# Kernel tuning notes

Measured on AMD Instinct MI355X. Metric: run time of the kernel, lower is better.

## Reference

```python
import jax, jax.numpy as jnp
import numpy as np

B, S, D = 4, 2048, 1024

def setup_inputs() -> dict:
    key = jax.random.key(0)
    k1, k2, k3, k4 = jax.random.split(key, 4)
    x = jax.random.normal(k1, (B, S, D), dtype=jnp.float32)
    # module init: jr.normal(key, (dim, dim)) / 40
    Qw = jax.random.normal(k2, (D, D), dtype=jnp.float32) / 40
    Kw = jax.random.normal(k3, (D, D), dtype=jnp.float32) / 40
    Vw = jax.random.normal(k4, (D, D), dtype=jnp.float32) / 40
    return {"x": x, "Qw": Qw, "Kw": Kw, "Vw": Vw}

def reference(x, Qw, Kw, Vw):
    # Q/K/V projections: [B,S,D] @ [D,D] -> [B,S,D]
    Q = x @ Qw
    K = x @ Kw
    V = x @ Vw
    d = x.shape[-1]
    S_len = x.shape[-2]
    # causal additive mask: 0 on/below diagonal, -inf above
    mask = jnp.where(jnp.tril(jnp.ones((S_len, S_len), dtype=x.dtype)) == 0,
                     -jnp.inf, 0.0).astype(x.dtype)
    # scores: [B,S,S]
    scores = jnp.einsum('bqd,bkd->bqk', Q, K) / jnp.sqrt(jnp.asarray(d, x.dtype))
    scores = scores + mask
    attn = jax.nn.softmax(scores, axis=-1)
    return jnp.einsum('bqk,bkd->bqd', attn, V)
```

## Files before the change

### kernel.cpp

```cpp
#include <hip/hip_runtime.h>
#include <hip/hip_bf16.h>

typedef __attribute__((ext_vector_type(8))) __bf16 bf16x8;
typedef __attribute__((ext_vector_type(8))) short short8;
typedef __attribute__((ext_vector_type(4))) float f32x4;

#define BM 128
#define BN 128
#define BK 64

__device__ inline unsigned short f2bf(float f) {
    union { float f; unsigned u; } v; v.f = f;
    unsigned r = (v.u + 0x7FFFu + ((v.u >> 16) & 1u)) >> 16;
    return (unsigned short)r;
}

__device__ __forceinline__ void gld16(const void* g, void* l) {
    __builtin_amdgcn_global_load_lds(
        (const __attribute__((address_space(1))) unsigned int*)g,
        (__attribute__((address_space(3))) unsigned int*)l, 16, 0, 0);
}

__global__ void detect_dtype(const unsigned short* __restrict__ x, int* __restrict__ flag)
{
    const int tid = threadIdx.x;
    int cnt = 0;
    for (int i = tid; i < 1024; i += 256) {
        unsigned e = (x[2 * i] >> 7) & 0xFFu;
        cnt += (e >= 0x60u && e <= 0x88u) ? 1 : 0;
    }
    #pragma unroll
    for (int o = 32; o >= 1; o >>= 1) cnt += __shfl_xor(cnt, o, 64);
    __shared__ int red[4];
    if ((tid & 63) == 0) red[tid >> 6] = cnt;
    __syncthreads();
    if (tid == 0) {
        int t = red[0] + red[1] + red[2] + red[3];
        *flag = (t >= 512) ? 0 : 1;
    }
}

__global__ __launch_bounds__(256, 2)
void gemm_bt(const unsigned short* __restrict__ A, const unsigned short* __restrict__ Bt,
             void* __restrict__ Call, int K, int lda, int ldb, int ldc,
             long oA, long oB, long oC, long sA, long sB, long sC,
             float scale, int mode, int q0,
             const int* __restrict__ dtf, int outKind)
{
    const int dt = *dtf;
    const int z = blockIdx.z;
    const long aBase = oA + (long)z * sA;
    const long bBase = oB + (long)z * sB;
    const long cBase = oC + (long)z * sC;

    int mt, nt;
    if (mode == 2) {
        const int nwg2 = gridDim.x * gridDim.y;
        const int h = blockIdx.y * gridDim.x + blockIdx.x;
        const int u = h >> 1;
        const int rank = (h & 1) ? (nwg2 - 1 - u) : u;
        mt = (gridDim.y - 1) - (rank / (int)gridDim.x);
        nt = rank % (int)gridDim.x;
    } else {
        const int nwg = gridDim.x * gridDim.y;
        int lin = blockIdx.y * gridDim.x + blockIdx.x;
        const int q = nwg >> 3, r = nwg & 7;
        const int xcd = lin & 7, idx = lin >> 3;
        lin = (xcd < r ? xcd * (q + 1) : r * (q + 1) + (xcd - r) * q) + idx;
        if (mode == 1) {
            int rem = lin, rr = 0, w = q0 / BN + 1;
            while (rem >= w) { rem -= w; rr++; w++; }
            mt = rr; nt = rem;
        } else { mt = lin / gridDim.x; nt = lin % gridDim.x; }
    }
    const int m0 = mt * BM;
    const int n0 = nt * BN;
    int kmax = K;
    if (mode == 2) kmax = min(K, q0 + m0 + BM);

    __shared__ __align__(16) short As[2][BM * BK];
    __shared__ __align__(16) short Bs[2][BN * BK];

    const int tid  = threadIdx.x;
    const int wave = tid >> 6;
    const int lane = tid & 63;
    const int wm = (wave >> 1) * 64;
    const int wn = (wave & 1) * 64;
    const int lrow = lane & 15;
    const int quad = lane >> 4;

    const int sRow = lane >> 3;
    const int sCol = ((lane & 7) ^ sRow) * 8;
    const long gA = aBase + (long)(m0 + wave * 32 + sRow) * lda + sCol;
    const long gB = bBase + (long)(n0 + wave * 32 + sRow) * ldb + sCol;

    auto stage = [&](int buf, int k0) {
        short* dA = &As[buf][wave * 32 * BK];
        short* dB = &Bs[buf][wave * 32 * BK];
        const unsigned short* pA = A + gA + k0;
        const unsigned short* pB = Bt + gB + k0;
        #pragma unroll
        for (int c = 0; c < 4; c++) {
            gld16(pA + (long)(c * 8) * lda, dA + c * 8 * BK);
            gld16(pB + (long)(c * 8) * ldb, dB + c * 8 * BK);
        }
    };

    f32x4 acc[4][4];
    #pragma unroll
    for (int i = 0; i < 4; i++)
        #pragma unroll
        for (int j = 0; j < 4; j++) {
            f32x4 zero = {0.f, 0.f, 0.f, 0.f};
            acc[i][j] = zero;
        }

    const int rq  = lrow & 7;
    const int pc0 = (quad ^ rq) * 8;
    const int pc1 = ((quad + 4) ^ rq) * 8;

    stage(0, 0);
    __syncthreads();
    int cur = 0;

    for (int k0 = 0; k0 < kmax; k0 += BK) {
        const int kn = k0 + BK;
        if (kn < kmax) stage(cur ^ 1, kn);

        const short* rA = &As[cur][0];
        const short* rB = &Bs[cur][0];
        bf16x8 af[4], bfr[4];
        #pragma unroll
        for (int i = 0; i < 4; i++) {
            af[i]  = *(const bf16x8*)&rA[(wm + i * 16 + lrow) * BK + pc0];
            bfr[i] = *(const bf16x8*)&rB[(wn + i * 16 + lrow) * BK + pc0];
        }
        #pragma unroll
        for (int i = 0; i < 4; i++)
            #pragma unroll
            for (int j = 0; j < 4; j++)
                acc[i][j] = __builtin_amdgcn_mfma_f32_16x16x32_bf16(af[i], bfr[j], acc[i][j], 0, 0, 0);
        #pragma unroll
        for (int i = 0; i < 4; i++) {
            af[i]  = *(const bf16x8*)&rA[(wm + i * 16 + lrow) * BK + pc1];
            bfr[i] = *(const bf16x8*)&rB[(wn + i * 16 + lrow) * BK + pc1];
        }
        #pragma unroll
        for (int i = 0; i < 4; i++)
            #pragma unroll
            for (int j = 0; j < 4; j++)
                acc[i][j] = __builtin_amdgcn_mfma_f32_16x16x32_bf16(af[i], bfr[j], acc[i][j], 0, 0, 0);

        __syncthreads();
        cur ^= 1;
    }

    const int oF32 = (outKind == 1) | ((outKind == 2) & dt);
    #pragma unroll
    for (int i = 0; i < 4; i++) {
        const int mr = m0 + wm + i * 16 + quad * 4;
        #pragma unroll
        for (int j = 0; j < 4; j++) {
            const int nc = n0 + wn + j * 16 + lrow;
            #pragma unroll
            for (int r = 0; r < 4; r++) {
                const long ofs = cBase + (long)(mr + r) * ldc + nc;
                const float v = acc[i][j][r] * scale;
                if (oF32) ((float*)Call)[ofs] = v;
                else      ((unsigned short*)Call)[ofs] = f2bf(v);
            }
        }
    }
}

__global__ __launch_bounds__(256)
void xpose_cast(const void* __restrict__ src, unsigned short* __restrict__ dT,
                unsigned short* __restrict__ dC, int R, int C,
                long oS, long sS, long sDT, long sDC,
                const int* __restrict__ dtf, int srcExt)
{
    const int dt = srcExt ? *dtf : 0;
    const int b = blockIdx.z;
    const long sb = oS + (long)b * sS;
    __shared__ unsigned short t[64][65];
    const int c0 = blockIdx.x * 64, r0 = blockIdx.y * 64;
    const int tid = threadIdx.x;
    #pragma unroll
    for (int it = 0; it < 16; it++) {
        int idx = it * 256 + tid;
        int r = idx >> 6, c = idx & 63;
        long e = sb + (long)(r0 + r) * C + (c0 + c);
        unsigned short v = dt ? f2bf(((const float*)src)[e]) : ((const unsigned short*)src)[e];
        t[r][c] = v;
        if (dC) dC[(long)b * sDC + (long)(r0 + r) * C + (c0 + c)] = v;
    }
    if (!dT) return;
    __syncthreads();
    #pragma unroll
    for (int it = 0; it < 16; it++) {
        int idx = it * 256 + tid;
        int r = idx >> 6, c = idx & 63;
        dT[(long)b * sDT + (long)(c0 + r) * R + (r0 + c)] = t[c][r];
    }
}

__global__ __launch_bounds__(256)
void cast2(const void* __restrict__ s0, const void* __restrict__ s1,
           unsigned short* __restrict__ d0, unsigned short* __restrict__ d1,
           long n, const int* __restrict__ dtf)
{
    const int dt = *dtf;
    const void* s = blockIdx.y ? s1 : s0;
    unsigned short* d = blockIdx.y ? d1 : d0;
    long i = ((long)blockIdx.x * 256 + threadIdx.x) * 8;
    if (i >= n) return;
    union { short8 v; unsigned short u[8]; } o;
    if (dt) {
        f32x4 a = *(const f32x4*)((const float*)s + i);
        f32x4 b = *(const f32x4*)((const float*)s + i + 4);
        #pragma unroll
        for (int j = 0; j < 4; j++) { o.u[j] = f2bf(a[j]); o.u[4 + j] = f2bf(b[j]); }
    } else {
        o.v = *(const short8*)((const short*)s + i);
    }
    *(short8*)(d + i) = o.v;
}

__global__ __launch_bounds__(256)
void softmax_causal(float* __restrict__ Sc, int S, int CH, int q0)
{
    const int r = blockIdx.x, z = blockIdx.y;
    float* srow = Sc + ((long)z * CH + r) * S;
    unsigned short* prow = (unsigned short*)srow;
    const int n = q0 + r + 1;
    const int limit = q0 + (r & ~(BM - 1)) + BM;
    const int tid = threadIdx.x;
    const int lane = tid & 63, wave = tid >> 6;
    __shared__ float red[4];

    float v[8];
    float lm = -1e30f;
    #pragma unroll
    for (int c = 0; c < 8; c++) {
        int j = c * 256 + tid;
        v[c] = (j < n) ? srow[j] : -1e30f;
        lm = fmaxf(lm, v[c]);
    }
    #pragma unroll
    for (int o = 32; o >= 1; o >>= 1) lm = fmaxf(lm, __shfl_xor(lm, o, 64));
    if (lane == 0) red[wave] = lm;
    __syncthreads();
    const float m = fmaxf(fmaxf(red[0], red[1]), fmaxf(red[2], red[3]));
    __syncthreads();

    float ev[8];
    float ls = 0.f;
    #pragma unroll
    for (int c = 0; c < 8; c++) {
        int j = c * 256 + tid;
        float e = (j < n) ? __expf(v[c] - m) : 0.f;
        ev[c] = e;
        ls += e;
    }
    #pragma unroll
    for (int o = 32; o >= 1; o >>= 1) ls += __shfl_xor(ls, o, 64);
    if (lane == 0) red[wave] = ls;
    __syncthreads();
    const float inv = 1.0f / (red[0] + red[1] + red[2] + red[3]);

    #pragma unroll
    for (int c = 0; c < 8; c++) {
        int j = c * 256 + tid;
        if (j < limit) prow[j] = f2bf(j < n ? ev[c] * inv : 0.f);
    }
}

__global__ __launch_bounds__(256)
void fill_zero(void* o, long n, const int* dtf)
{
    long i = (long)blockIdx.x * 256 + threadIdx.x;
    if (i < n) {
        if (*dtf) ((float*)o)[i] = 0.f;
        else ((unsigned short*)o)[i] = 0;
    }
}

extern "C" void kernel_launch(void* const* d_in, const int* in_sizes, int n_in,
                              void* d_out, int out_size, void* d_ws, size_t ws_size,
                              hipStream_t stream)
{
    const int B = 4, S = 2048, D = 1024;
    const void* x  = d_in[0];
    const void* Qw = d_in[1];
    const void* Kw = d_in[2];
    const void* Vw = d_in[3];
    (void)in_sizes; (void)n_in; (void)out_size;

    int* dtf = (int*)d_ws;
    char* p = (char*)d_ws + 4096;
    const size_t MB = (size_t)1 << 20;

    detect_dtype<<<1, 256, 0, stream>>>((const unsigned short*)x, dtf);

    const long nOut = (long)B * S * D;

    const size_t needA = 4096 + 36 * MB + (size_t)B * S * S * 4;
    if (ws_size >= needA) {
        unsigned short* QwB = (unsigned short*)p;
        unsigned short* KwB = (unsigned short*)(p + 2 * MB);
        unsigned short* Xb  = (unsigned short*)(p + 4 * MB);
        unsigned short* Buf = (unsigned short*)(p + 20 * MB);
        float* Sc = (float*)(p + 36 * MB);
        unsigned short* WT  = (unsigned short*)Sc;
        unsigned short* VwT = QwB;
        unsigned short* VbT = Xb;

        xpose_cast<<<dim3(16, 32, 4), 256, 0, stream>>>(
            x, nullptr, Xb, S, D, 0L, (long)S * D, 0L, (long)S * D, dtf, 1);
        cast2<<<dim3(512, 2), 256, 0, stream>>>(Qw, Kw, QwB, KwB, (long)D * D, dtf);
        gemm_bt<<<dim3(8, 8, 1), 256, 0, stream>>>(
            KwB, QwB, WT, D, D, D, D, 0L, 0L, 0L, 0L, 0L, 0L, 0.03125f, 0, 0, dtf, 0);
        gemm_bt<<<dim3(8, 64, 1), 256, 0, stream>>>(
            Xb, WT, Buf, D, D, D, D, 0L, 0L, 0L, 0L, 0L, 0L, 1.0f, 0, 0, dtf, 0);
        gemm_bt<<<dim3(136, 1, 4), 256, 0, stream>>>(
            Buf, Xb, (void*)Sc, D, D, D, S,
            0L, 0L, 0L, (long)S * D, (long)S * D, (long)S * S, 1.0f, 1, 0, dtf, 1);
        softmax_causal<<<dim3(S, 4), 256, 0, stream>>>(Sc, S, S, 0);
        xpose_cast<<<dim3(16, 16, 1), 256, 0, stream>>>(
            Vw, VwT, nullptr, D, D, 0L, 0L, 0L, 0L, dtf, 1);
        gemm_bt<<<dim3(8, 64, 1), 256, 0, stream>>>(
            Xb, VwT, Buf, D, D, D, D, 0L, 0L, 0L, 0L, 0L, 0L, 1.0f, 0, 0, dtf, 0);
        xpose_cast<<<dim3(16, 32, 4), 256, 0, stream>>>(
            Buf, VbT, nullptr, S, D, 0L, (long)S * D, (long)D * S, 0L, dtf, 0);
        gemm_bt<<<dim3(8, 16, 4), 256, 0, stream>>>(
            (const unsigned short*)Sc, VbT, d_out, S, 2 * S, S, D,
            0L, 0L, 0L, (long)2 * S * S, (long)D * S, (long)S * D, 1.0f, 2, 0, dtf, 2);
        return;
    }

    const int cfgs[6][2] = {{4,1024},{2,1024},{1,1024},{1,512},{1,256},{1,128}};
    int ZB = 0, CH = 0;
    for (int i = 0; i < 6; i++) {
        size_t need = 4096 + 56 * MB + (size_t)cfgs[i][0] * cfgs[i][1] * S * 4;
        if (need <= ws_size) { ZB = cfgs[i][0]; CH = cfgs[i][1]; break; }
    }
    if (ZB == 0) {
        fill_zero<<<dim3((unsigned)((nOut + 255) / 256)), 256, 0, stream>>>(d_out, nOut, dtf);
        return;
    }

    unsigned short* QwB = (unsigned short*)p;
    unsigned short* KwB = (unsigned short*)(p + 2 * MB);
    unsigned short* WT  = (unsigned short*)(p + 4 * MB);
    unsigned short* VwT = (unsigned short*)(p + 6 * MB);
    unsigned short* Xb  = (unsigned short*)(p + 8 * MB);
    unsigned short* VbT = (unsigned short*)(p + 24 * MB);
    unsigned short* Buf = (unsigned short*)(p + 40 * MB);
    float* Sc = (float*)(p + 56 * MB);
    unsigned short* VbS = (unsigned short*)d_out;

    xpose_cast<<<dim3(16, 32, 4), 256, 0, stream>>>(
        x, nullptr, Xb, S, D, 0L, (long)S * D, 0L, (long)S * D, dtf, 1);
    cast2<<<dim3(512, 2), 256, 0, stream>>>(Qw, Kw, QwB, KwB, (long)D * D, dtf);
    xpose_cast<<<dim3(16, 16, 1), 256, 0, stream>>>(Vw, VwT, nullptr, D, D, 0L, 0L, 0L, 0L, dtf, 1);

    gemm_bt<<<dim3(8, 8, 1), 256, 0, stream>>>(
        KwB, QwB, WT, D, D, D, D, 0L, 0L, 0L, 0L, 0L, 0L, 0.03125f, 0, 0, dtf, 0);
    gemm_bt<<<dim3(8, 64, 1), 256, 0, stream>>>(
        Xb, WT, Buf, D, D, D, D, 0L, 0L, 0L, 0L, 0L, 0L, 1.0f, 0, 0, dtf, 0);
    gemm_bt<<<dim3(8, 64, 1), 256, 0, stream>>>(
        Xb, VwT, VbS, D, D, D, D, 0L, 0L, 0L, 0L, 0L, 0L, 1.0f, 0, 0, dtf, 0);
    xpose_cast<<<dim3(16, 32, 4), 256, 0, stream>>>(
        VbS, VbT, nullptr, S, D, 0L, (long)S * D, (long)D * S, 0L, dtf, 0);

    for (int b0 = 0; b0 < B; b0 += ZB) {
        for (int q0 = 0; q0 < S; q0 += CH) {
            const int base = q0 / BN, R = CH / BM;
            const int ntiles = R * (base + 1) + R * (R - 1) / 2;

            gemm_bt<<<dim3(ntiles, 1, ZB), 256, 0, stream>>>(
                Buf, Xb, (void*)Sc, D, D, D, S,
                (long)b0 * S * D + (long)q0 * D, (long)b0 * S * D, 0L,
                (long)S * D, (long)S * D, (long)CH * S, 1.0f, 1, q0, dtf, 1);

            softmax_causal<<<dim3(CH, ZB), 256, 0, stream>>>(Sc, S, CH, q0);

            gemm_bt<<<dim3(8, CH / BM, ZB), 256, 0, stream>>>(
                (const unsigned short*)Sc, VbT, d_out, S, 2 * S, S, D,
                0L, (long)b0 * D * S, (long)b0 * S * D + (long)q0 * D,
                (long)CH * 2 * S, (long)D * S, (long)S * D, 1.0f, 2, q0, dtf, 2);
        }
    }
}
```

Measured before the change: 282.9 us.

## Template GEMM tile size, halve BK, and batch Q/V projections in one launch

Templates the GEMM on tile size, so the small weight-product GEMM runs with 64x64 tiles for more workgroups, and reduces the K-step from 64 to 32 with a new LDS swizzle. Raises the occupancy hint to 4 workgroups per CU, since smaller LDS buffers allow it. Merges the Xb@WT and Xb@VwT projections into one launch using grid z to pick the second weight and output. The smaller K-step means twice as many barriers per K and less MFMA work between them, which could hurt the large GEMMs.

```diff
diff --git a/kernel.cpp b/kernel.cpp
--- a/kernel.cpp
+++ b/kernel.cpp
@@ -5,9 +5,7 @@
 typedef __attribute__((ext_vector_type(8))) short short8;
 typedef __attribute__((ext_vector_type(4))) float f32x4;
 
-#define BM 128
-#define BN 128
-#define BK 64
+#define BK 32
 
 __device__ inline unsigned short f2bf(float f) {
     union { float f; unsigned u; } v; v.f = f;
@@ -40,15 +38,19 @@
     }
 }
 
-__global__ __launch_bounds__(256, 2)
+template <int TM>
+__global__ __launch_bounds__(256, 4)
 void gemm_bt(const unsigned short* __restrict__ A, const unsigned short* __restrict__ Bt,
              void* __restrict__ Call, int K, int lda, int ldb, int ldc,
              long oA, long oB, long oC, long sA, long sB, long sC,
              float scale, int mode, int q0,
-             const int* __restrict__ dtf, int outKind)
-{
+             const int* __restrict__ dtf, int outKind,
+             const unsigned short* __restrict__ Bt2, void* __restrict__ C2)
+{
+    constexpr int NI = TM / 32;
     const int dt = *dtf;
     const int z = blockIdx.z;
+    if (Bt2 && z) { Bt = Bt2; Call = C2; }
     const long aBase = oA + (long)z * sA;
     const long bBase = oB + (long)z * sB;
     const long cBase = oC + (long)z * sC;
@@ -68,56 +70,54 @@
         const int xcd = lin & 7, idx = lin >> 3;
         lin = (xcd < r ? xcd * (q + 1) : r * (q + 1) + (xcd - r) * q) + idx;
         if (mode == 1) {
-            int rem = lin, rr = 0, w = q0 / BN + 1;
+            int rem = lin, rr = 0, w = q0 / TM + 1;
             while (rem >= w) { rem -= w; rr++; w++; }
             mt = rr; nt = rem;
         } else { mt = lin / gridDim.x; nt = lin % gridDim.x; }
     }
-    const int m0 = mt * BM;
-    const int n0 = nt * BN;
+    const int m0 = mt * TM;
+    const int n0 = nt * TM;
     int kmax = K;
-    if (mode == 2) kmax = min(K, q0 + m0 + BM);
-
-    __shared__ __align__(16) short As[2][BM * BK];
-    __shared__ __align__(16) short Bs[2][BN * BK];
+    if (mode == 2) kmax = min(K, q0 + m0 + TM);
+
+    __shared__ __align__(16) short As[2][TM * BK];
+    __shared__ __align__(16) short Bs[2][TM * BK];
 
     const int tid  = threadIdx.x;
     const int wave = tid >> 6;
     const int lane = tid & 63;
-    const int wm = (wave >> 1) * 64;
-    const int wn = (wave & 1) * 64;
+    const int wm = (wave >> 1) * (TM / 2);
+    const int wn = (wave & 1) * (TM / 2);
     const int lrow = lane & 15;
     const int quad = lane >> 4;
 
-    const int sRow = lane >> 3;
-    const int sCol = ((lane & 7) ^ sRow) * 8;
-    const long gA = aBase + (long)(m0 + wave * 32 + sRow) * lda + sCol;
-    const long gB = bBase + (long)(n0 + wave * 32 + sRow) * ldb + sCol;
+    const int sRow = lane >> 2;
+    const int sCol = ((lane & 3) ^ ((lane >> 3) & 3)) * 8;
+    const long gA = aBase + (long)(m0 + wave * (TM / 4) + sRow) * lda + sCol;
+    const long gB = bBase + (long)(n0 + wave * (TM / 4) + sRow) * ldb + sCol;
 
     auto stage = [&](int buf, int k0) {
-        short* dA = &As[buf][wave * 32 * BK];
-        short* dB = &Bs[buf][wave * 32 * BK];
+        short* dA = &As[buf][wave * (TM / 4) * BK];
+        short* dB = &Bs[buf][wave * (TM / 4) * BK];
         const unsigned short* pA = A + gA + k0;
         const unsigned short* pB = Bt + gB + k0;
         #pragma unroll
-        for (int c = 0; c < 4; c++) {
-            gld16(pA + (long)(c * 8) * lda, dA + c * 8 * BK);
-            gld16(pB + (long)(c * 8) * ldb, dB + c * 8 * BK);
+        for (int c = 0; c < TM / 64; c++) {
+            gld16(pA + (long)(c * 16) * lda, dA + c * 16 * BK);
+            gld16(pB + (long)(c * 16) * ldb, dB + c * 16 * BK);
         }
     };
 
-    f32x4 acc[4][4];
-    #pragma unroll
-    for (int i = 0; i < 4; i++)
-        #pragma unroll
-        for (int j = 0; j < 4; j++) {
+    f32x4 acc[NI][NI];
+    #pragma unroll
+    for (int i = 0; i < NI; i++)
+        #pragma unroll
+        for (int j = 0; j < NI; j++) {
             f32x4 zero = {0.f, 0.f, 0.f, 0.f};
             acc[i][j] = zero;
         }
 
-    const int rq  = lrow & 7;
-    const int pc0 = (quad ^ rq) * 8;
-    const int pc1 = ((quad + 4) ^ rq) * 8;
+    const int pc = (quad ^ ((lrow >> 1) & 3)) * 8;
 
     stage(0, 0);
     __syncthreads();
@@ -129,26 +129,16 @@
 
         const short* rA = &As[cur][0];
         const short* rB = &Bs[cur][0];
-        bf16x8 af[4], bfr[4];
-        #pragma unroll
-        for (int i = 0; i < 4; i++) {
-            af[i]  = *(const bf16x8*)&rA[(wm + i * 16 + lrow) * BK + pc0];
-            bfr[i] = *(const bf16x8*)&rB[(wn + i * 16 + lrow) * BK + pc0];
-        }
-        #pragma unroll
-        for (int i = 0; i < 4; i++)
+        bf16x8 af[NI], bfr[NI];
+        #pragma unroll
+        for (int i = 0; i < NI; i++) {
+            af[i]  = *(const bf16x8*)&rA[(wm + i * 16 + lrow) * BK + pc];
+            bfr[i] = *(const bf16x8*)&rB[(wn + i * 16 + lrow) * BK + pc];
+        }
+        #pragma unroll
+        for (int i = 0; i < NI; i++)
             #pragma unroll
-            for (int j = 0; j < 4; j++)
-                acc[i][j] = __builtin_amdgcn_mfma_f32_16x16x32_bf16(af[i], bfr[j], acc[i][j], 0, 0, 0);
-        #pragma unroll
-        for (int i = 0; i < 4; i++) {
-            af[i]  = *(const bf16x8*)&rA[(wm + i * 16 + lrow) * BK + pc1];
-            bfr[i] = *(const bf16x8*)&rB[(wn + i * 16 + lrow) * BK + pc1];
-        }
-        #pragma unroll
-        for (int i = 0; i < 4; i++)
-            #pragma unroll
-            for (int j = 0; j < 4; j++)
+            for (int j = 0; j < NI; j++)
                 acc[i][j] = __builtin_amdgcn_mfma_f32_16x16x32_bf16(af[i], bfr[j], acc[i][j], 0, 0, 0);
 
         __syncthreads();
@@ -157,10 +147,10 @@
 
     const int oF32 = (outKind == 1) | ((outKind == 2) & dt);
     #pragma unroll
-    for (int i = 0; i < 4; i++) {
+    for (int i = 0; i < NI; i++) {
         const int mr = m0 + wm + i * 16 + quad * 4;
         #pragma unroll
-        for (int j = 0; j < 4; j++) {
+        for (int j = 0; j < NI; j++) {
             const int nc = n0 + wn + j * 16 + lrow;
             #pragma unroll
             for (int r = 0; r < 4; r++) {
@@ -233,7 +223,7 @@
     float* srow = Sc + ((long)z * CH + r) * S;
     unsigned short* prow = (unsigned short*)srow;
     const int n = q0 + r + 1;
-    const int limit = q0 + (r & ~(BM - 1)) + BM;
+    const int limit = q0 + (r & ~127) + 128;
     const int tid = threadIdx.x;
     const int lane = tid & 63, wave = tid >> 6;
     __shared__ float red[4];
@@ -299,6 +289,7 @@
     int* dtf = (int*)d_ws;
     char* p = (char*)d_ws + 4096;
     const size_t MB = (size_t)1 << 20;
+    const unsigned short* nullB = nullptr;
 
     detect_dtype<<<1, 256, 0, stream>>>((const unsigned short*)x, dtf);
 
@@ -314,27 +305,30 @@
         unsigned short* WT  = (unsigned short*)Sc;
         unsigned short* VwT = QwB;
         unsigned short* VbT = Xb;
+        unsigned short* VbS = (unsigned short*)d_out;
 
         xpose_cast<<<dim3(16, 32, 4), 256, 0, stream>>>(
             x, nullptr, Xb, S, D, 0L, (long)S * D, 0L, (long)S * D, dtf, 1);
         cast2<<<dim3(512, 2), 256, 0, stream>>>(Qw, Kw, QwB, KwB, (long)D * D, dtf);
-        gemm_bt<<<dim3(8, 8, 1), 256, 0, stream>>>(
-            KwB, QwB, WT, D, D, D, D, 0L, 0L, 0L, 0L, 0L, 0L, 0.03125f, 0, 0, dtf, 0);
-        gemm_bt<<<dim3(8, 64, 1), 256, 0, stream>>>(
-            Xb, WT, Buf, D, D, D, D, 0L, 0L, 0L, 0L, 0L, 0L, 1.0f, 0, 0, dtf, 0);
-        gemm_bt<<<dim3(136, 1, 4), 256, 0, stream>>>(
-            Buf, Xb, (void*)Sc, D, D, D, S,
-            0L, 0L, 0L, (long)S * D, (long)S * D, (long)S * S, 1.0f, 1, 0, dtf, 1);
-        softmax_causal<<<dim3(S, 4), 256, 0, stream>>>(Sc, S, S, 0);
+        gemm_bt<64><<<dim3(16, 16, 1), 256, 0, stream>>>(
+            KwB, QwB, WT, D, D, D, D, 0L, 0L, 0L, 0L, 0L, 0L,
+            0.03125f, 0, 0, dtf, 0, nullB, nullptr);
         xpose_cast<<<dim3(16, 16, 1), 256, 0, stream>>>(
             Vw, VwT, nullptr, D, D, 0L, 0L, 0L, 0L, dtf, 1);
-        gemm_bt<<<dim3(8, 64, 1), 256, 0, stream>>>(
-            Xb, VwT, Buf, D, D, D, D, 0L, 0L, 0L, 0L, 0L, 0L, 1.0f, 0, 0, dtf, 0);
+        gemm_bt<128><<<dim3(8, 64, 2), 256, 0, stream>>>(
+            Xb, WT, Buf, D, D, D, D, 0L, 0L, 0L, 0L, 0L, 0L,
+            1.0f, 0, 0, dtf, 0, VwT, VbS);
+        gemm_bt<128><<<dim3(136, 1, 4), 256, 0, stream>>>(
+            Buf, Xb, (void*)Sc, D, D, D, S,
+            0L, 0L, 0L, (long)S * D, (long)S * D, (long)S * S,
+            1.0f, 1, 0, dtf, 1, nullB, nullptr);
+        softmax_causal<<<dim3(S, 4), 256, 0, stream>>>(Sc, S, S, 0);
         xpose_cast<<<dim3(16, 32, 4), 256, 0, stream>>>(
-            Buf, VbT, nullptr, S, D, 0L, (long)S * D, (long)D * S, 0L, dtf, 0);
-        gemm_bt<<<dim3(8, 16, 4), 256, 0, stream>>>(
+            VbS, VbT, nullptr, S, D, 0L, (long)S * D, (long)D * S, 0L, dtf, 0);
+        gemm_bt<128><<<dim3(8, 16, 4), 256, 0, stream>>>(
             (const unsigned short*)Sc, VbT, d_out, S, 2 * S, S, D,
-            0L, 0L, 0L, (long)2 * S * S, (long)D * S, (long)S * D, 1.0f, 2, 0, dtf, 2);
+            0L, 0L, 0L, (long)2 * S * S, (long)D * S, (long)S * D,
+            1.0f, 2, 0, dtf, 2, nullB, nullptr);
         return;
     }
 
@@ -364,31 +358,33 @@
     cast2<<<dim3(512, 2), 256, 0, stream>>>(Qw, Kw, QwB, KwB, (long)D * D, dtf);
     xpose_cast<<<dim3(16, 16, 1), 256, 0, stream>>>(Vw, VwT, nullptr, D, D, 0L, 0L, 0L, 0L, dtf, 1);
 
-    gemm_bt<<<dim3(8, 8, 1), 256, 0, stream>>>(
-        KwB, QwB, WT, D, D, D, D, 0L, 0L, 0L, 0L, 0L, 0L, 0.03125f, 0, 0, dtf, 0);
-    gemm_bt<<<dim3(8, 64, 1), 256, 0, stream>>>(
-        Xb, WT, Buf, D, D, D, D, 0L, 0L, 0L, 0L, 0L, 0L, 1.0f, 0, 0, dtf, 0);
-    gemm_bt<<<dim3(8, 64, 1), 256, 0, stream>>>(
-        Xb, VwT, VbS, D, D, D, D, 0L, 0L, 0L, 0L, 0L, 0L, 1.0f, 0, 0, dtf, 0);
+    gemm_bt<64><<<dim3(16, 16, 1), 256, 0, stream>>>(
+        KwB, QwB, WT, D, D, D, D, 0L, 0L, 0L, 0L, 0L, 0L,
+        0.03125f, 0, 0, dtf, 0, nullB, nullptr);
+    gemm_bt<128><<<dim3(8, 64, 2), 256, 0, stream>>>(
+        Xb, WT, Buf, D, D, D, D, 0L, 0L, 0L, 0L, 0L, 0L,
+        1.0f, 0, 0, dtf, 0, VwT, VbS);
     xpose_cast<<<dim3(16, 32, 4), 256, 0, stream>>>(
         VbS, VbT, nullptr, S, D, 0L, (long)S * D, (long)D * S, 0L, dtf, 0);
 
     for (int b0 = 0; b0 < B; b0 += ZB) {
         for (int q0 = 0; q0 < S; q0 += CH) {
-            const int base = q0 / BN, R = CH / BM;
+            const int base = q0 / 128, R = CH / 128;
             const int ntiles = R * (base + 1) + R * (R - 1) / 2;
 
-            gemm_bt<<<dim3(ntiles, 1, ZB), 256, 0, stream>>>(
+            gemm_bt<128><<<dim3(ntiles, 1, ZB), 256, 0, stream>>>(
                 Buf, Xb, (void*)Sc, D, D, D, S,
                 (long)b0 * S * D + (long)q0 * D, (long)b0 * S * D, 0L,
-                (long)S * D, (long)S * D, (long)CH * S, 1.0f, 1, q0, dtf, 1);
+                (long)S * D, (long)S * D, (long)CH * S,
+                1.0f, 1, q0, dtf, 1, nullB, nullptr);
 
             softmax_causal<<<dim3(CH, ZB), 256, 0, stream>>>(Sc, S, CH, q0);
 
-            gemm_bt<<<dim3(8, CH / BM, ZB), 256, 0, stream>>>(
+            gemm_bt<128><<<dim3(8, CH / 128, ZB), 256, 0, stream>>>(
                 (const unsigned short*)Sc, VbT, d_out, S, 2 * S, S, D,
                 0L, (long)b0 * D * S, (long)b0 * S * D + (long)q0 * D,
-                (long)CH * 2 * S, (long)D * S, (long)S * D, 1.0f, 2, q0, dtf, 2);
-        }
-    }
-}
+                (long)CH * 2 * S, (long)D * S, (long)S * D,
+                1.0f, 2, q0, dtf, 2, nullB, nullptr);
+        }
+    }
+}
```

Measured after the change: 272.7 us. 1.04x faster.
